# Optimization experiments

Hardware: AMD Instinct MI355X
Metric: run time of the kernel (lower is better)

Reference implementation:

```python
import jax, jax.numpy as jnp
import numpy as np

B, T, DIM, HEADS, DH = 4, 2048, 1024, 16, 64
MAX_SEQ_LEN = 2048


def setup_inputs() -> dict:
    key = jax.random.key(0)
    k1, k2, k3, k4 = jax.random.split(key, 4)
    x = jax.random.normal(k1, (B, T, DIM), dtype=jnp.float32)
    W_qkv = jax.random.normal(k2, (DIM, 3 * HEADS * DH), dtype=jnp.float32) * (DIM ** -0.5)
    W_0 = jax.random.normal(k3, (HEADS * DH, DIM), dtype=jnp.float32) * ((HEADS * DH) ** -0.5)
    rel_bias = jax.random.normal(k4, (2 * MAX_SEQ_LEN - 1, HEADS), dtype=jnp.float32) * 0.02
    return {"x": x, "W_qkv": W_qkv, "W_0": W_0, "rel_bias": rel_bias}


def reference(x, W_qkv, W_0, rel_bias):
    b, t, dim = x.shape
    heads = rel_bias.shape[1]
    dh = W_qkv.shape[1] // (3 * heads)
    scale = dh ** -0.5

    qkv = x @ W_qkv  # (b, t, 3*heads*dh), feature layout is (d, k, h): d slowest, h fastest
    qkv = qkv.reshape(b, t, dh, 3, heads)
    qkv = jnp.transpose(qkv, (3, 0, 4, 1, 2))  # (3, b, h, t, d)
    q, k, v = qkv[0], qkv[1], qkv[2]

    scores = jnp.einsum('bhid,bhjd->bhij', q, k) * scale  # (b, h, t, t)

    causal = jnp.tril(jnp.ones((t, t), dtype=bool))
    scores = jnp.where(causal[None, None], scores, -jnp.inf)

    # relative position bias: index = j - i + t - 1
    rel_idx = jnp.arange(t)[None, :] - jnp.arange(t)[:, None] + (t - 1)  # (t, t)
    bias = rel_bias[rel_idx]  # (t, t, heads)
    scores = scores + jnp.transpose(bias, (2, 0, 1))[None]

    attn = jax.nn.softmax(scores, axis=-1)
    out = jnp.einsum('bhij,bhjd->bhid', attn, v)  # (b, h, t, d)
    out = jnp.transpose(out, (0, 2, 1, 3)).reshape(b, t, heads * dh)
    return out @ W_0
```

## Files before the change

### kernel.cpp

```cpp
#include <hip/hip_runtime.h>
#include <hip/hip_bf16.h>
#include <stdint.h>

#define B_ 4
#define T_ 2048
#define NH 16
#define DH 64
#define DIM 1024
#define NF 3072

typedef unsigned short u16;
typedef uint32_t u32;
typedef __bf16 bf16;
typedef bf16 bf16x8 __attribute__((ext_vector_type(8)));
typedef float f32x4 __attribute__((ext_vector_type(4)));
typedef u16 u16x8 __attribute__((ext_vector_type(8)));
typedef u16 u16x4 __attribute__((ext_vector_type(4)));

__device__ __forceinline__ u16 f2bf(float f) {
    u32 u = __builtin_bit_cast(u32, f);
    u = (u + 0x7fffu + ((u >> 16) & 1u)) >> 16;
    return (u16)u;
}

__device__ __forceinline__ float exp2f_fast(float x) {
#if __has_builtin(__builtin_amdgcn_exp2f)
    return __builtin_amdgcn_exp2f(x);
#else
    return exp2f(x);
#endif
}

#define GLOAD16(g, l)                                                          \
    __builtin_amdgcn_global_load_lds(                                          \
        (const __attribute__((address_space(1))) u32*)(g),                     \
        (__attribute__((address_space(3))) u32*)(l), 16, 0, 0)


__global__ __launch_bounds__(256) void cvt_bf16_k(const float* __restrict__ src,
                                                  u16* __restrict__ dst, int n8) {
    int i = blockIdx.x * 256 + threadIdx.x;
    if (i >= n8) return;
    const float4* s = (const float4*)src + (size_t)i * 2;
    float4 a = s[0], b = s[1];
    u16x8 o;
    o[0]=f2bf(a.x); o[1]=f2bf(a.y); o[2]=f2bf(a.z); o[3]=f2bf(a.w);
    o[4]=f2bf(b.x); o[5]=f2bf(b.y); o[6]=f2bf(b.z); o[7]=f2bf(b.w);
    *(u16x8*)(dst + (size_t)i * 8) = o;
}

template <int PERM>
__global__ __launch_bounds__(256) void wcvt_t_k(const float* __restrict__ src,
                                                u16* __restrict__ dst, int K, int N) {
    __shared__ float tile[32][33];
    int n0 = blockIdx.x * 32, k0 = blockIdx.y * 32;
    int c = threadIdx.x & 31, r0 = threadIdx.x >> 5;
#pragma unroll
    for (int i = 0; i < 4; i++) {
        int r = r0 + i * 8;
        tile[r][c] = src[(size_t)(k0 + r) * N + n0 + c];
    }
    __syncthreads();
#pragma unroll
    for (int i = 0; i < 4; i++) {
        int r = r0 + i * 8;
        int n = n0 + r;
        int nd;
        if (PERM) {
            int d = n / 48, rem = n - d * 48;
            int kk = rem >> 4, h = rem & 15;
            nd = kk * 1024 + h * 64 + d;
        } else {
            nd = n;
        }
        dst[(size_t)nd * K + k0 + c] = f2bf(tile[c][r]);
    }
}

__global__ __launch_bounds__(256) void rbt_k(const float* __restrict__ rb,
                                             u16* __restrict__ rbT2,
                                             u16* __restrict__ rbT2s) {
    int i = blockIdx.x * 256 + threadIdx.x;
    if (i >= NH * 4096) return;
    int h = i >> 12, d = i & 4095;
    float v = (d <= 2047) ? rb[(size_t)d * NH + h] * 1.44269504f : -1e30f;
    rbT2[i] = __builtin_bit_cast(u16, (bf16)v);
    int d2 = d + 1;
    float v2 = (d2 <= 2047) ? rb[(size_t)d2 * NH + h] * 1.44269504f : -1e30f;
    rbT2s[i] = __builtin_bit_cast(u16, (bf16)v2);
}

__global__ __launch_bounds__(256) void transpose_v_k(const u16* __restrict__ qkvF,
                                                     u16* __restrict__ Vt) {
    __shared__ __align__(16) u16 tile[64][72];
    int bh = blockIdx.y;
    int h = bh & 15, b = bh >> 4;
    int t0 = blockIdx.x * 64;
    const u16* src = qkvF + ((size_t)b * T_ + t0) * NF + 2048 + h * 64;
    for (int idx = threadIdx.x; idx < 512; idx += 256) {
        int r = idx >> 3, ch = idx & 7;
        *(u16x8*)&tile[r][ch * 8] = *(const u16x8*)&src[(size_t)r * NF + ch * 8];
    }
    __syncthreads();
    u16* dst = Vt + (size_t)bh * DH * T_ + t0;
    for (int idx = threadIdx.x; idx < 512; idx += 256) {
        int d = idx >> 3, ch = idx & 7;
        u16x8 v;
#pragma unroll
        for (int e = 0; e < 8; e++) v[e] = tile[ch * 8 + e][d];
        *(u16x8*)&dst[(size_t)d * T_ + ch * 8] = v;
    }
}


template <int WRITE_BF16>
__global__ __launch_bounds__(256, 2) void gemm_bt_k(const u16* __restrict__ A,
                                                    const u16* __restrict__ Bt,
                                                    void* __restrict__ Cout,
                                                    int M, int N, int K) {
    __shared__ __align__(16) u16 As[128 * 32];
    __shared__ __align__(16) u16 Bs[128 * 32];
    const int tid = threadIdx.x;
    const int wave = tid >> 6, lane = tid & 63;
    const int bm = blockIdx.x, bn = blockIdx.y;
    const int wr = (wave >> 1) * 64, wc = (wave & 1) * 64;
    const int lrow = lane & 15, lk = (lane >> 4) * 8;
    const int srow = lane >> 2;
    const int sk = (lane & 3) * 8;
    const u16* Ab = A + (size_t)(bm * 128 + wave * 32) * K;
    const u16* Bb = Bt + (size_t)(bn * 128 + wave * 32) * K;
    u16* AsW = As + wave * 1024;
    u16* BsW = Bs + wave * 1024;
    f32x4 acc[4][4] = {};

    for (int k0 = 0; k0 < K; k0 += 32) {
        __syncthreads();
        GLOAD16(Ab + (size_t)srow * K + k0 + sk, AsW);
        GLOAD16(Ab + (size_t)(srow + 16) * K + k0 + sk, AsW + 512);
        GLOAD16(Bb + (size_t)srow * K + k0 + sk, BsW);
        GLOAD16(Bb + (size_t)(srow + 16) * K + k0 + sk, BsW + 512);
        __syncthreads();
        bf16x8 af[4], bfr[4];
#pragma unroll
        for (int i = 0; i < 4; i++) af[i] = *(const bf16x8*)&As[(wr + i * 16 + lrow) * 32 + lk];
#pragma unroll
        for (int j = 0; j < 4; j++) bfr[j] = *(const bf16x8*)&Bs[(wc + j * 16 + lrow) * 32 + lk];
#pragma unroll
        for (int i = 0; i < 4; i++)
#pragma unroll
            for (int j = 0; j < 4; j++)
                acc[i][j] = __builtin_amdgcn_mfma_f32_16x16x32_bf16(af[i], bfr[j], acc[i][j], 0, 0, 0);
    }

    const int crow = (lane >> 4) * 4, ccol = lane & 15;
#pragma unroll
    for (int i = 0; i < 4; i++)
#pragma unroll
        for (int j = 0; j < 4; j++) {
            int gm = bm * 128 + wr + i * 16 + crow;
            int gn = bn * 128 + wc + j * 16 + ccol;
#pragma unroll
            for (int r = 0; r < 4; r++) {
                if (WRITE_BF16)
                    ((u16*)Cout)[(size_t)(gm + r) * N + gn] = f2bf(acc[i][j][r]);
                else
                    ((float*)Cout)[(size_t)(gm + r) * N + gn] = acc[i][j][r];
            }
        }
}

__global__ __launch_bounds__(256, 2) void flash_attn_k(const u16* __restrict__ qkvF,
                                                       const u16* __restrict__ Vt,
                                                       const u16* __restrict__ rbT2,
                                                       const u16* __restrict__ rbT2s,
                                                       u16* __restrict__ O) {
    __shared__ __align__(16) u16 Ks[64 * 64];
    __shared__ __align__(16) u16 Vs[64 * 64];
    __shared__ __align__(16) u16 Ps[4][2][16 * 64];
    __shared__ __align__(16) u16 rbs2a[4096];
    __shared__ __align__(16) u16 rbs2b[4096];
    const int tid = threadIdx.x, wave = tid >> 6, lane = tid & 63;
    const int Lid = blockIdx.x;
    const int c = Lid & 7, u = Lid >> 3;
    const int bh = ((u & 7) << 3) | c;
    const int pair = u >> 3;
    const int h = bh & 15, b = bh >> 4;
    const int l15 = lane & 15, g4 = lane >> 4;
    const float SC2 = 0.125f * 1.44269504f;

    {
        *(u16x8*)&rbs2a[tid * 8] = *(const u16x8*)&rbT2[(size_t)h * 4096 + tid * 8];
        *(u16x8*)&rbs2a[2048 + tid * 8] = *(const u16x8*)&rbT2[(size_t)h * 4096 + 2048 + tid * 8];
        *(u16x8*)&rbs2b[tid * 8] = *(const u16x8*)&rbT2s[(size_t)h * 4096 + tid * 8];
        *(u16x8*)&rbs2b[2048 + tid * 8] = *(const u16x8*)&rbT2s[(size_t)h * 4096 + 2048 + tid * 8];
    }

    const size_t trow = (size_t)b * T_;
    const int srow = tid >> 2;
    const int sch = tid & 3;
    u16* pwA = &Ps[wave][0][0];
    u16* pwB = &Ps[wave][1][0];
    const u16* kgb = &qkvF[(trow + srow) * NF + 1024 + h * 64];
    const u16* vgb = &Vt[((size_t)bh * DH + srow) * T_];

    u16x8 kv0 = *(const u16x8*)&kgb[sch * 8];
    u16x8 kv1 = *(const u16x8*)&kgb[(sch + 4) * 8];
    u16x8 vv0 = *(const u16x8*)&vgb[sch * 8];
    u16x8 vv1 = *(const u16x8*)&vgb[(sch + 4) * 8];

    for (int half = 0; half < 2; half++) {
        const int blk = half ? 15 - pair : pair;
        const int qbA = blk * 128 + wave * 16;
        const int qbB = qbA + 64;
        bf16x8 aqA[2], aqB[2];
        aqA[0] = *(const bf16x8*)&qkvF[(trow + qbA + l15) * NF + h * 64 + g4 * 8];
        aqA[1] = *(const bf16x8*)&qkvF[(trow + qbA + l15) * NF + h * 64 + 32 + g4 * 8];
        aqB[0] = *(const bf16x8*)&qkvF[(trow + qbB + l15) * NF + h * 64 + g4 * 8];
        aqB[1] = *(const bf16x8*)&qkvF[(trow + qbB + l15) * NF + h * 64 + 32 + g4 * 8];

        const int ibA = 2047 - l15 + g4 * 4 - qbA;
        const u32* b32A = (const u32*)((ibA & 1) ? &rbs2b[ibA - 1] : &rbs2a[ibA]);
        const u32* b32B = b32A - 32;

        f32x4 oaccA[4] = {}, oaccB[4] = {};
        float lA = 0.f, lB = 0.f;

        const int jtmax = 2 * blk + 1;
        for (int jt = 0; jt <= jtmax; jt++) {
            const int j0 = jt * 64;
            __syncthreads();
            {
                int sw = srow & 7;
                *(u16x8*)&Ks[srow * 64 + ((sch ^ sw) * 8)] = kv0;
                *(u16x8*)&Ks[srow * 64 + (((sch + 4) ^ sw) * 8)] = kv1;
                *(u16x8*)&Vs[srow * 64 + ((sch ^ sw) * 8)] = vv0;
                *(u16x8*)&Vs[srow * 64 + (((sch + 4) ^ sw) * 8)] = vv1;
            }
            __syncthreads();
            {
                int njt = jt + 1;
                int j0n = (njt <= jtmax) ? njt * 64 : (half == 0 ? 0 : -1);
                if (j0n >= 0) {
                    const u16* kg = kgb + (size_t)j0n * NF;
                    const u16* vg = vgb + j0n;
                    kv0 = *(const u16x8*)&kg[sch * 8];
                    kv1 = *(const u16x8*)&kg[(sch + 4) * 8];
                    vv0 = *(const u16x8*)&vg[sch * 8];
                    vv1 = *(const u16x8*)&vg[(sch + 4) * 8];
                }
            }
            f32x4 sA[4], sB[4];
#pragma unroll
            for (int ni = 0; ni < 4; ni++) {
                f32x4 z = {};
                sA[ni] = z;
                sB[ni] = z;
            }
            __builtin_amdgcn_s_setprio(1);
#pragma unroll
            for (int ni = 0; ni < 4; ni++) {
                int arow = ni * 16 + l15;
#pragma unroll
                for (int kk = 0; kk < 2; kk++) {
                    int ch = kk * 4 + g4;
                    bf16x8 ak = *(const bf16x8*)&Ks[arow * 64 + ((ch ^ (arow & 7)) * 8)];
                    sA[ni] = __builtin_amdgcn_mfma_f32_16x16x32_bf16(ak, aqA[kk], sA[ni], 0, 0, 0);
                    sB[ni] = __builtin_amdgcn_mfma_f32_16x16x32_bf16(ak, aqB[kk], sB[ni], 0, 0, 0);
                }
            }
            __builtin_amdgcn_s_setprio(0);
            const int jo = j0 >> 1;
            {
                float su = 0.f;
#pragma unroll
                for (int ni = 0; ni < 4; ni++) {
                    u32 w0 = b32A[jo + ni * 8];
                    u32 w1 = b32A[jo + ni * 8 + 1];
                    float e0 = exp2f_fast(fmaf(sA[ni][0], SC2, __builtin_bit_cast(float, w0 << 16)));
                    float e1 = exp2f_fast(fmaf(sA[ni][1], SC2, __builtin_bit_cast(float, w0 & 0xffff0000u)));
                    float e2 = exp2f_fast(fmaf(sA[ni][2], SC2, __builtin_bit_cast(float, w1 << 16)));
                    float e3 = exp2f_fast(fmaf(sA[ni][3], SC2, __builtin_bit_cast(float, w1 & 0xffff0000u)));
                    su += (e0 + e1) + (e2 + e3);
                    u16x4 pk;
                    pk[0] = __builtin_bit_cast(u16, (bf16)e0);
                    pk[1] = __builtin_bit_cast(u16, (bf16)e1);
                    pk[2] = __builtin_bit_cast(u16, (bf16)e2);
                    pk[3] = __builtin_bit_cast(u16, (bf16)e3);
                    int colb = ni * 16 + g4 * 4;
                    int ch = colb >> 3, co = colb & 7;
                    *(u16x4*)&pwA[l15 * 64 + ((ch ^ (l15 & 7)) * 8) + co] = pk;
                }
                su += __shfl_xor(su, 16);
                su += __shfl_xor(su, 32);
                lA += su;
            }
            {
                float su = 0.f;
#pragma unroll
                for (int ni = 0; ni < 4; ni++) {
                    u32 w0 = b32B[jo + ni * 8];
                    u32 w1 = b32B[jo + ni * 8 + 1];
                    float e0 = exp2f_fast(fmaf(sB[ni][0], SC2, __builtin_bit_cast(float, w0 << 16)));
                    float e1 = exp2f_fast(fmaf(sB[ni][1], SC2, __builtin_bit_cast(float, w0 & 0xffff0000u)));
                    float e2 = exp2f_fast(fmaf(sB[ni][2], SC2, __builtin_bit_cast(float, w1 << 16)));
                    float e3 = exp2f_fast(fmaf(sB[ni][3], SC2, __builtin_bit_cast(float, w1 & 0xffff0000u)));
                    su += (e0 + e1) + (e2 + e3);
                    u16x4 pk;
                    pk[0] = __builtin_bit_cast(u16, (bf16)e0);
                    pk[1] = __builtin_bit_cast(u16, (bf16)e1);
                    pk[2] = __builtin_bit_cast(u16, (bf16)e2);
                    pk[3] = __builtin_bit_cast(u16, (bf16)e3);
                    int colb = ni * 16 + g4 * 4;
                    int ch = colb >> 3, co = colb & 7;
                    *(u16x4*)&pwB[l15 * 64 + ((ch ^ (l15 & 7)) * 8) + co] = pk;
                }
                su += __shfl_xor(su, 16);
                su += __shfl_xor(su, 32);
                lB += su;
            }
            bf16x8 bpA[2], bpB[2];
#pragma unroll
            for (int kk = 0; kk < 2; kk++) {
                int ch = kk * 4 + g4;
                int off = l15 * 64 + ((ch ^ (l15 & 7)) * 8);
                bpA[kk] = *(const bf16x8*)&pwA[off];
                bpB[kk] = *(const bf16x8*)&pwB[off];
            }
            __builtin_amdgcn_s_setprio(1);
#pragma unroll
            for (int di = 0; di < 4; di++) {
                int vrow = di * 16 + l15;
#pragma unroll
                for (int kk = 0; kk < 2; kk++) {
                    int ch = kk * 4 + g4;
                    bf16x8 av = *(const bf16x8*)&Vs[vrow * 64 + ((ch ^ (vrow & 7)) * 8)];
                    oaccA[di] = __builtin_amdgcn_mfma_f32_16x16x32_bf16(av, bpA[kk], oaccA[di], 0, 0, 0);
                    oaccB[di] = __builtin_amdgcn_mfma_f32_16x16x32_bf16(av, bpB[kk], oaccB[di], 0, 0, 0);
                }
            }
            __builtin_amdgcn_s_setprio(0);
        }
        {
            float inv = 1.0f / lA;
            u16* orow = &O[((size_t)b * T_ + qbA + l15) * (NH * DH) + h * DH];
#pragma unroll
            for (int di = 0; di < 4; di++) {
                u16x4 ov;
#pragma unroll
                for (int r = 0; r < 4; r++)
                    ov[r] = __builtin_bit_cast(u16, (bf16)(oaccA[di][r] * inv));
                *(u16x4*)&orow[di * 16 + g4 * 4] = ov;
            }
        }
        {
            float inv = 1.0f / lB;
            u16* orow = &O[((size_t)b * T_ + qbB + l15) * (NH * DH) + h * DH];
#pragma unroll
            for (int di = 0; di < 4; di++) {
                u16x4 ov;
#pragma unroll
                for (int r = 0; r < 4; r++)
                    ov[r] = __builtin_bit_cast(u16, (bf16)(oaccB[di][r] * inv));
                *(u16x4*)&orow[di * 16 + g4 * 4] = ov;
            }
        }
    }
}


extern "C" void kernel_launch(void* const* d_in, const int* in_sizes, int n_in,
                              void* d_out, int out_size, void* d_ws, size_t ws_size,
                              hipStream_t stream) {
    const float* x    = (const float*)d_in[0];
    const float* Wqkv = (const float*)d_in[1];
    const float* W0   = (const float*)d_in[2];
    const float* rb   = (const float*)d_in[3];
    char* ws = (char*)d_ws;

    u16*   xb    = (u16*)(ws + 0);
    u16*   WqkvT = (u16*)(ws + 16777216);
    u16*   W0T   = (u16*)(ws + 23068672);
    u16*   rbT2  = (u16*)(ws + 25165824);
    u16*   rbT2s = (u16*)(ws + 25296896);
    u16*   qkvF  = (u16*)(ws + 25559040);
    u16*   attnO = (u16*)(ws + 75890688);
    u16*   Vtb   = (u16*)(ws + 0);

    cvt_bf16_k<<<4096, 256, 0, stream>>>(x, xb, (B_ * T_ * DIM) / 8);
    wcvt_t_k<1><<<dim3(NF / 32, DIM / 32), 256, 0, stream>>>(Wqkv, WqkvT, DIM, NF);
    wcvt_t_k<0><<<dim3(DIM / 32, DIM / 32), 256, 0, stream>>>(W0, W0T, DIM, DIM);
    rbt_k<<<(NH * 4096 + 255) / 256, 256, 0, stream>>>(rb, rbT2, rbT2s);

    gemm_bt_k<1><<<dim3((B_ * T_) / 128, NF / 128), 256, 0, stream>>>(
        xb, WqkvT, qkvF, B_ * T_, NF, DIM);

    transpose_v_k<<<dim3(T_ / 64, B_ * NH), 256, 0, stream>>>(qkvF, Vtb);

    flash_attn_k<<<512, 256, 0, stream>>>(qkvF, Vtb, rbT2, rbT2s, attnO);

    gemm_bt_k<0><<<dim3((B_ * T_) / 128, DIM / 128), 256, 0, stream>>>(
        attnO, W0T, d_out, B_ * T_, DIM, DIM);
}
```

Measured before the change: 188.6 us.

## Deepen GEMM K-tile with swizzled LDS and read fp32 bias from global

The GEMM now stages a K-step of 64 instead of 32, with an XOR-swizzled LDS layout, which halves the number of barrier pairs and is meant to reduce bank conflicts. In the attention kernel, the bf16 relative-bias tables in shared memory are replaced by four shifted fp32 copies in global memory, read as aligned float4 loads per tile. This frees LDS, which may allow more occupancy, and gives full-precision bias values. The cost is extra global/L2 traffic inside the inner loop and larger shared-memory tiles in the GEMM.

```diff
diff --git a/kernel.cpp b/kernel.cpp
--- a/kernel.cpp
+++ b/kernel.cpp
@@ -8,6 +8,7 @@
 #define DH 64
 #define DIM 1024
 #define NF 3072
+#define TBL 4112
 
 typedef unsigned short u16;
 typedef uint32_t u32;
@@ -78,16 +79,14 @@
 }
 
 __global__ __launch_bounds__(256) void rbt_k(const float* __restrict__ rb,
-                                             u16* __restrict__ rbT2,
-                                             u16* __restrict__ rbT2s) {
+                                             float* __restrict__ rbF4) {
     int i = blockIdx.x * 256 + threadIdx.x;
-    if (i >= NH * 4096) return;
-    int h = i >> 12, d = i & 4095;
-    float v = (d <= 2047) ? rb[(size_t)d * NH + h] * 1.44269504f : -1e30f;
-    rbT2[i] = __builtin_bit_cast(u16, (bf16)v);
-    int d2 = d + 1;
-    float v2 = (d2 <= 2047) ? rb[(size_t)d2 * NH + h] * 1.44269504f : -1e30f;
-    rbT2s[i] = __builtin_bit_cast(u16, (bf16)v2);
+    if (i >= 4 * NH * TBL) return;
+    int s = i / (NH * TBL);
+    int rem = i - s * (NH * TBL);
+    int h = rem / TBL, d = rem - h * TBL;
+    int d2 = d + s;
+    rbF4[i] = (d2 <= 2047) ? rb[(size_t)d2 * NH + h] * 1.44269504f : -1e30f;
 }
 
 __global__ __launch_bounds__(256) void transpose_v_k(const u16* __restrict__ qkvF,
@@ -118,38 +117,47 @@
                                                     const u16* __restrict__ Bt,
                                                     void* __restrict__ Cout,
                                                     int M, int N, int K) {
-    __shared__ __align__(16) u16 As[128 * 32];
-    __shared__ __align__(16) u16 Bs[128 * 32];
+    __shared__ __align__(16) u16 As[128 * 64];
+    __shared__ __align__(16) u16 Bs[128 * 64];
     const int tid = threadIdx.x;
     const int wave = tid >> 6, lane = tid & 63;
     const int bm = blockIdx.x, bn = blockIdx.y;
     const int wr = (wave >> 1) * 64, wc = (wave & 1) * 64;
-    const int lrow = lane & 15, lk = (lane >> 4) * 8;
-    const int srow = lane >> 2;
-    const int sk = (lane & 3) * 8;
+    const int lrow = lane & 15, g4 = lane >> 4;
+    const int srow8 = lane >> 3;
+    const int scs = (lane & 7) ^ srow8;
     const u16* Ab = A + (size_t)(bm * 128 + wave * 32) * K;
     const u16* Bb = Bt + (size_t)(bn * 128 + wave * 32) * K;
-    u16* AsW = As + wave * 1024;
-    u16* BsW = Bs + wave * 1024;
+    u16* AsW = As + wave * 2048;
+    u16* BsW = Bs + wave * 2048;
     f32x4 acc[4][4] = {};
 
-    for (int k0 = 0; k0 < K; k0 += 32) {
+    for (int k0 = 0; k0 < K; k0 += 64) {
         __syncthreads();
-        GLOAD16(Ab + (size_t)srow * K + k0 + sk, AsW);
-        GLOAD16(Ab + (size_t)(srow + 16) * K + k0 + sk, AsW + 512);
-        GLOAD16(Bb + (size_t)srow * K + k0 + sk, BsW);
-        GLOAD16(Bb + (size_t)(srow + 16) * K + k0 + sk, BsW + 512);
+#pragma unroll
+        for (int g = 0; g < 4; g++) {
+            GLOAD16(Ab + (size_t)(g * 8 + srow8) * K + k0 + scs * 8, AsW + g * 512);
+            GLOAD16(Bb + (size_t)(g * 8 + srow8) * K + k0 + scs * 8, BsW + g * 512);
+        }
         __syncthreads();
-        bf16x8 af[4], bfr[4];
-#pragma unroll
-        for (int i = 0; i < 4; i++) af[i] = *(const bf16x8*)&As[(wr + i * 16 + lrow) * 32 + lk];
-#pragma unroll
-        for (int j = 0; j < 4; j++) bfr[j] = *(const bf16x8*)&Bs[(wc + j * 16 + lrow) * 32 + lk];
-#pragma unroll
-        for (int i = 0; i < 4; i++)
+#pragma unroll
+        for (int kk2 = 0; kk2 < 2; kk2++) {
+            bf16x8 af[4], bfr[4];
+#pragma unroll
+            for (int i = 0; i < 4; i++)
+                af[i] = *(const bf16x8*)&As[(wr + i * 16 + lrow) * 64 +
+                                            (((kk2 * 4 + g4) ^ (lrow & 7)) * 8)];
 #pragma unroll
             for (int j = 0; j < 4; j++)
-                acc[i][j] = __builtin_amdgcn_mfma_f32_16x16x32_bf16(af[i], bfr[j], acc[i][j], 0, 0, 0);
+                bfr[j] = *(const bf16x8*)&Bs[(wc + j * 16 + lrow) * 64 +
+                                             (((kk2 * 4 + g4) ^ (lrow & 7)) * 8)];
+#pragma unroll
+            for (int i = 0; i < 4; i++)
+#pragma unroll
+                for (int j = 0; j < 4; j++)
+                    acc[i][j] = __builtin_amdgcn_mfma_f32_16x16x32_bf16(af[i], bfr[j],
+                                                                        acc[i][j], 0, 0, 0);
+        }
     }
 
     const int crow = (lane >> 4) * 4, ccol = lane & 15;
@@ -171,14 +179,11 @@
 
 __global__ __launch_bounds__(256, 2) void flash_attn_k(const u16* __restrict__ qkvF,
                                                        const u16* __restrict__ Vt,
-                                                       const u16* __restrict__ rbT2,
-                                                       const u16* __restrict__ rbT2s,
+                                                       const float* __restrict__ rbF,
                                                        u16* __restrict__ O) {
     __shared__ __align__(16) u16 Ks[64 * 64];
     __shared__ __align__(16) u16 Vs[64 * 64];
     __shared__ __align__(16) u16 Ps[4][2][16 * 64];
-    __shared__ __align__(16) u16 rbs2a[4096];
-    __shared__ __align__(16) u16 rbs2b[4096];
     const int tid = threadIdx.x, wave = tid >> 6, lane = tid & 63;
     const int Lid = blockIdx.x;
     const int c = Lid & 7, u = Lid >> 3;
@@ -187,13 +192,6 @@
     const int h = bh & 15, b = bh >> 4;
     const int l15 = lane & 15, g4 = lane >> 4;
     const float SC2 = 0.125f * 1.44269504f;
-
-    {
-        *(u16x8*)&rbs2a[tid * 8] = *(const u16x8*)&rbT2[(size_t)h * 4096 + tid * 8];
-        *(u16x8*)&rbs2a[2048 + tid * 8] = *(const u16x8*)&rbT2[(size_t)h * 4096 + 2048 + tid * 8];
-        *(u16x8*)&rbs2b[tid * 8] = *(const u16x8*)&rbT2s[(size_t)h * 4096 + tid * 8];
-        *(u16x8*)&rbs2b[2048 + tid * 8] = *(const u16x8*)&rbT2s[(size_t)h * 4096 + 2048 + tid * 8];
-    }
 
     const size_t trow = (size_t)b * T_;
     const int srow = tid >> 2;
@@ -218,9 +216,10 @@
         aqB[0] = *(const bf16x8*)&qkvF[(trow + qbB + l15) * NF + h * 64 + g4 * 8];
         aqB[1] = *(const bf16x8*)&qkvF[(trow + qbB + l15) * NF + h * 64 + 32 + g4 * 8];
 
-        const int ibA = 2047 - l15 + g4 * 4 - qbA;
-        const u32* b32A = (const u32*)((ibA & 1) ? &rbs2b[ibA - 1] : &rbs2a[ibA]);
-        const u32* b32B = b32A - 32;
+        const int ib0 = 2047 - l15 + g4 * 4 - qbA;
+        const int sA = ib0 & 3;
+        const float* bgA = rbF + ((size_t)(sA * NH + h)) * TBL + (ib0 - sA);
+        const float* bgB = bgA - 64;
 
         f32x4 oaccA[4] = {}, oaccB[4] = {};
         float lA = 0.f, lB = 0.f;
@@ -249,12 +248,18 @@
                     vv1 = *(const u16x8*)&vg[(sch + 4) * 8];
                 }
             }
-            f32x4 sA[4], sB[4];
+            float4 bqA[4], bqB[4];
+#pragma unroll
+            for (int ni = 0; ni < 4; ni++) {
+                bqA[ni] = *(const float4*)&bgA[j0 + ni * 16];
+                bqB[ni] = *(const float4*)&bgB[j0 + ni * 16];
+            }
+            f32x4 sA_[4], sB_[4];
 #pragma unroll
             for (int ni = 0; ni < 4; ni++) {
                 f32x4 z = {};
-                sA[ni] = z;
-                sB[ni] = z;
+                sA_[ni] = z;
+                sB_[ni] = z;
             }
             __builtin_amdgcn_s_setprio(1);
 #pragma unroll
@@ -264,22 +269,20 @@
                 for (int kk = 0; kk < 2; kk++) {
                     int ch = kk * 4 + g4;
                     bf16x8 ak = *(const bf16x8*)&Ks[arow * 64 + ((ch ^ (arow & 7)) * 8)];
-                    sA[ni] = __builtin_amdgcn_mfma_f32_16x16x32_bf16(ak, aqA[kk], sA[ni], 0, 0, 0);
-                    sB[ni] = __builtin_amdgcn_mfma_f32_16x16x32_bf16(ak, aqB[kk], sB[ni], 0, 0, 0);
+                    sA_[ni] = __builtin_amdgcn_mfma_f32_16x16x32_bf16(ak, aqA[kk], sA_[ni], 0, 0, 0);
+                    sB_[ni] = __builtin_amdgcn_mfma_f32_16x16x32_bf16(ak, aqB[kk], sB_[ni], 0, 0, 0);
                 }
             }
             __builtin_amdgcn_s_setprio(0);
-            const int jo = j0 >> 1;
             {
                 float su = 0.f;
 #pragma unroll
                 for (int ni = 0; ni < 4; ni++) {
-                    u32 w0 = b32A[jo + ni * 8];
-                    u32 w1 = b32A[jo + ni * 8 + 1];
-                    float e0 = exp2f_fast(fmaf(sA[ni][0], SC2, __builtin_bit_cast(float, w0 << 16)));
-                    float e1 = exp2f_fast(fmaf(sA[ni][1], SC2, __builtin_bit_cast(float, w0 & 0xffff0000u)));
-                    float e2 = exp2f_fast(fmaf(sA[ni][2], SC2, __builtin_bit_cast(float, w1 << 16)));
-                    float e3 = exp2f_fast(fmaf(sA[ni][3], SC2, __builtin_bit_cast(float, w1 & 0xffff0000u)));
+                    const float* bb = (const float*)&bqA[ni];
+                    float e0 = exp2f_fast(fmaf(sA_[ni][0], SC2, bb[0]));
+                    float e1 = exp2f_fast(fmaf(sA_[ni][1], SC2, bb[1]));
+                    float e2 = exp2f_fast(fmaf(sA_[ni][2], SC2, bb[2]));
+                    float e3 = exp2f_fast(fmaf(sA_[ni][3], SC2, bb[3]));
                     su += (e0 + e1) + (e2 + e3);
                     u16x4 pk;
                     pk[0] = __builtin_bit_cast(u16, (bf16)e0);
@@ -298,12 +301,11 @@
                 float su = 0.f;
 #pragma unroll
                 for (int ni = 0; ni < 4; ni++) {
-                    u32 w0 = b32B[jo + ni * 8];
-                    u32 w1 = b32B[jo + ni * 8 + 1];
-                    float e0 = exp2f_fast(fmaf(sB[ni][0], SC2, __builtin_bit_cast(float, w0 << 16)));
-                    float e1 = exp2f_fast(fmaf(sB[ni][1], SC2, __builtin_bit_cast(float, w0 & 0xffff0000u)));
-                    float e2 = exp2f_fast(fmaf(sB[ni][2], SC2, __builtin_bit_cast(float, w1 << 16)));
-                    float e3 = exp2f_fast(fmaf(sB[ni][3], SC2, __builtin_bit_cast(float, w1 & 0xffff0000u)));
+                    const float* bb = (const float*)&bqB[ni];
+                    float e0 = exp2f_fast(fmaf(sB_[ni][0], SC2, bb[0]));
+                    float e1 = exp2f_fast(fmaf(sB_[ni][1], SC2, bb[1]));
+                    float e2 = exp2f_fast(fmaf(sB_[ni][2], SC2, bb[2]));
+                    float e3 = exp2f_fast(fmaf(sB_[ni][3], SC2, bb[3]));
                     su += (e0 + e1) + (e2 + e3);
                     u16x4 pk;
                     pk[0] = __builtin_bit_cast(u16, (bf16)e0);
@@ -380,23 +382,22 @@
     u16*   xb    = (u16*)(ws + 0);
     u16*   WqkvT = (u16*)(ws + 16777216);
     u16*   W0T   = (u16*)(ws + 23068672);
-    u16*   rbT2  = (u16*)(ws + 25165824);
-    u16*   rbT2s = (u16*)(ws + 25296896);
-    u16*   qkvF  = (u16*)(ws + 25559040);
-    u16*   attnO = (u16*)(ws + 75890688);
+    float* rbF4  = (float*)(ws + 25165824);
+    u16*   qkvF  = (u16*)(ws + 26222592);
+    u16*   attnO = (u16*)(ws + 76554240);
     u16*   Vtb   = (u16*)(ws + 0);
 
     cvt_bf16_k<<<4096, 256, 0, stream>>>(x, xb, (B_ * T_ * DIM) / 8);
     wcvt_t_k<1><<<dim3(NF / 32, DIM / 32), 256, 0, stream>>>(Wqkv, WqkvT, DIM, NF);
     wcvt_t_k<0><<<dim3(DIM / 32, DIM / 32), 256, 0, stream>>>(W0, W0T, DIM, DIM);
-    rbt_k<<<(NH * 4096 + 255) / 256, 256, 0, stream>>>(rb, rbT2, rbT2s);
+    rbt_k<<<(4 * NH * TBL + 255) / 256, 256, 0, stream>>>(rb, rbF4);
 
     gemm_bt_k<1><<<dim3((B_ * T_) / 128, NF / 128), 256, 0, stream>>>(
         xb, WqkvT, qkvF, B_ * T_, NF, DIM);
 
     transpose_v_k<<<dim3(T_ / 64, B_ * NH), 256, 0, stream>>>(qkvF, Vtb);
 
-    flash_attn_k<<<512, 256, 0, stream>>>(qkvF, Vtb, rbT2, rbT2s, attnO);
+    flash_attn_k<<<512, 256, 0, stream>>>(qkvF, Vtb, rbF4, attnO);
 
     gemm_bt_k<0><<<dim3((B_ * T_) / 128, DIM / 128), 256, 0, stream>>>(
         attnO, W0T, d_out, B_ * T_, DIM, DIM);
```

After: 192.9 us. 2.3% more time.
